# Optimization experiments

Hardware: AMD Instinct MI355X
Metric: run time of the kernel (lower is better)

The kernel has to match this reference:

```python
import jax, jax.numpy as jnp
import numpy as np

# Qwen3MoeSparseMLPBlock config
T = 2048            # tokens
H = 2048            # hidden_size
I = 768             # moe_intermediate_size
E = 32              # num_experts
K = 8               # num_experts_per_tok
CAP = 1024          # per-expert capacity = 2 * (T*K/E); routing is ~uniform so never overflows


def setup_inputs() -> dict:
    key = jax.random.key(0)
    k1, k2, k3, k4, k5 = jax.random.split(key, 5)
    hidden_states = jax.random.normal(k1, (T, H), dtype=jnp.float32)
    gate_w = jax.random.normal(k2, (H, E), dtype=jnp.float32) / np.sqrt(H)
    gate_b = 0.01 * jax.random.normal(k3, (E,), dtype=jnp.float32)
    w_gate_up = jax.random.normal(k4, (E, H, 2 * I), dtype=jnp.float32) / np.sqrt(H)
    w_down = jax.random.normal(k5, (E, I, H), dtype=jnp.float32) / np.sqrt(I)
    return {"hidden_states": hidden_states, "gate_w": gate_w, "gate_b": gate_b,
            "w_gate_up": w_gate_up, "w_down": w_down}


def _moe(x, gate_w, gate_b, w_gate_up, w_down):
    # router: softmax in fp32, top-k, renormalize (norm_topk_prob=True)
    logits = x @ gate_w + gate_b                                   # [T, E]
    probs = jax.nn.softmax(logits.astype(jnp.float32), axis=-1)
    vals, idx = jax.lax.top_k(probs, K)                            # [T, K]
    vals = vals / jnp.sum(vals, axis=-1, keepdims=True)

    # token permutation: sort the T*K (token, expert) assignments by expert id
    A = T * K
    e_flat = idx.reshape(-1)                                       # [A] expert id per assignment
    t_flat = jnp.arange(A, dtype=jnp.int32) // K                   # [A] token id per assignment
    order = jnp.argsort(e_flat)                                    # assignments grouped by expert
    counts = jnp.bincount(e_flat, length=E)                        # [E] tokens per expert
    starts = jnp.cumsum(counts) - counts                           # [E] group offsets

    # fixed-capacity windows into the sorted assignment list (rows beyond count masked)
    win = jnp.minimum(starts[:, None] + jnp.arange(CAP)[None, :], A - 1)   # [E, CAP]
    valid = (jnp.arange(CAP)[None, :] < counts[:, None]).astype(x.dtype)   # [E, CAP]
    tok = t_flat[order][win]                                       # [E, CAP] source token ids
    w = vals.reshape(-1)[order][win] * valid                       # [E, CAP] routing weights (0 on pads)

    # gather -> grouped FFN (SiluAndMul) -> weighted scatter-add combine
    xb = x[tok]                                                    # [E, CAP, H]
    gu = jnp.einsum('ech,ehf->ecf', xb, w_gate_up)                 # [E, CAP, 2I]
    g, u = jnp.split(gu, 2, axis=-1)
    h = jax.nn.silu(g) * u                                         # [E, CAP, I]
    yb = jnp.einsum('eci,eih->ech', h, w_down) * w[..., None]      # [E, CAP, H]
    out = jnp.zeros_like(x).at[tok.reshape(-1)].add(yb.reshape(-1, H))
    return out


def reference(hidden_states, gate_w, gate_b, w_gate_up, w_down):
    return _moe(hidden_states, gate_w, gate_b, w_gate_up, w_down)
```

## Files before the change

### kernel.cpp

```cpp
#include <hip/hip_runtime.h>
#include <math.h>

#define TT 2048
#define HH 2048
#define ID 768
#define NE 32
#define KTOP 8
#define CAP 1024

typedef short bf16x8 __attribute__((ext_vector_type(8)));
typedef float f32x4 __attribute__((ext_vector_type(4)));

__device__ __forceinline__ unsigned short f2b(float f) {
  unsigned int u = __builtin_bit_cast(unsigned int, f);
  u += 0x7fff + ((u >> 16) & 1);
  return (unsigned short)(u >> 16);
}

__global__ __launch_bounds__(256) void cvt_x_kernel(const float* __restrict__ x,
                                                    unsigned short* __restrict__ xb) {
  const size_t i = ((size_t)blockIdx.x * 256 + threadIdx.x) * 8;
  const float4 a = *(const float4*)(x + i);
  const float4 b = *(const float4*)(x + i + 4);
  union { unsigned short us[8]; uint4 v; } p;
  p.us[0] = f2b(a.x); p.us[1] = f2b(a.y); p.us[2] = f2b(a.z); p.us[3] = f2b(a.w);
  p.us[4] = f2b(b.x); p.us[5] = f2b(b.y); p.us[6] = f2b(b.z); p.us[7] = f2b(b.w);
  *(uint4*)(xb + i) = p.v;
}

__global__ __launch_bounds__(256) void router_kernel(
    const float* __restrict__ x, const float* __restrict__ gw,
    const float* __restrict__ gb, int* __restrict__ counts,
    int* __restrict__ tok_slot, float* __restrict__ w_slot) {
  const int t = blockIdx.x;
  const int tid = threadIdx.x;
  const int e = tid & 31;
  const int c = tid >> 5;
  const float* xr = x + (size_t)t * HH;

  __shared__ double pl[8][NE];
  __shared__ float logits[NE];

  double a0 = 0.0, a1 = 0.0, a2 = 0.0, a3 = 0.0;
  const int j0 = c * 256;
#pragma unroll 4
  for (int j = 0; j < 256; j += 4) {
    const int jj = j0 + j;
    a0 = fma((double)xr[jj + 0], (double)gw[(size_t)(jj + 0) * NE + e], a0);
    a1 = fma((double)xr[jj + 1], (double)gw[(size_t)(jj + 1) * NE + e], a1);
    a2 = fma((double)xr[jj + 2], (double)gw[(size_t)(jj + 2) * NE + e], a2);
    a3 = fma((double)xr[jj + 3], (double)gw[(size_t)(jj + 3) * NE + e], a3);
  }
  pl[c][e] = (a0 + a1) + (a2 + a3);
  __syncthreads();

  if (tid < NE) {
    double s = 0.0;
    for (int cc = 0; cc < 8; ++cc) s += pl[cc][tid];
    logits[tid] = (float)s + gb[tid];
  }
  __syncthreads();

  if (tid == 0) {
    float l[NE];
    float m = -1e30f;
    for (int i = 0; i < NE; ++i) { l[i] = logits[i]; m = fmaxf(m, l[i]); }
    int sel[KTOP]; float ex[KTOP]; float s = 0.f;
    for (int k = 0; k < KTOP; ++k) {
      float best = -1e30f; int bi = 0;
      for (int i = 0; i < NE; ++i)
        if (l[i] > best) { best = l[i]; bi = i; }
      sel[k] = bi;
      ex[k] = expf(best - m);
      s += ex[k];
      l[bi] = -1e31f;
    }
    const float inv = 1.f / s;
    for (int k = 0; k < KTOP; ++k) {
      const int ee = sel[k];
      const int pos = atomicAdd(&counts[ee], 1);
      if (pos < CAP) {
        tok_slot[ee * CAP + pos] = t;
        w_slot[ee * CAP + pos] = ex[k] * inv;
      }
    }
  }
}

__global__ __launch_bounds__(256) void gu_kernel(
    const unsigned short* __restrict__ xb, const float* __restrict__ wgu,
    const int* __restrict__ counts, const int* __restrict__ tok_slot,
    unsigned short* __restrict__ h_ws) {
  const int e = blockIdx.z, mt = blockIdx.y, nt = blockIdx.x;
  int cnt = counts[e]; cnt = cnt > CAP ? CAP : cnt;
  if (mt * 128 >= cnt) return;

  __shared__ __align__(16) unsigned short As[128][40];
  __shared__ __align__(16) unsigned short Bg[64][40];
  __shared__ __align__(16) unsigned short Bu[64][40];
  __shared__ int toks[128];

  const int tid = threadIdx.x;
  if (tid < 128) toks[tid] = tok_slot[e * CAP + mt * 128 + tid];
  __syncthreads();

  const float* wg = wgu + (size_t)e * HH * (2 * ID) + nt * 64;
  const float* wu = wg + ID;

  const int wid = tid >> 6, lane = tid & 63;
  const int wm = wid & 1, wn = wid >> 1;
  const int lr = lane & 15, quad = lane >> 4;

  f32x4 accg[4][2], accu[4][2];
  for (int s = 0; s < 4; ++s)
    for (int t = 0; t < 2; ++t)
      for (int r = 0; r < 4; ++r) { accg[s][t][r] = 0.f; accu[s][t][r] = 0.f; }

  for (int k0 = 0; k0 < HH; k0 += 32) {
#pragma unroll
    for (int it = 0; it < 2; ++it) {
      const int task = tid + it * 256;
      const int row = task >> 2, cg = task & 3;
      const uint4 v = *(const uint4*)(xb + (size_t)toks[row] * HH + k0 + cg * 8);
      *(uint4*)&As[row][cg * 8] = v;
    }
#pragma unroll
    for (int it = 0; it < 2; ++it) {
      const int task = tid + it * 256;
      const int k = task >> 4, cg = task & 15;
      const size_t off = (size_t)(k0 + k) * (2 * ID) + cg * 4;
      const float4 vg = *(const float4*)(wg + off);
      const float4 vu = *(const float4*)(wu + off);
      Bg[cg * 4 + 0][k] = f2b(vg.x); Bg[cg * 4 + 1][k] = f2b(vg.y);
      Bg[cg * 4 + 2][k] = f2b(vg.z); Bg[cg * 4 + 3][k] = f2b(vg.w);
      Bu[cg * 4 + 0][k] = f2b(vu.x); Bu[cg * 4 + 1][k] = f2b(vu.y);
      Bu[cg * 4 + 2][k] = f2b(vu.z); Bu[cg * 4 + 3][k] = f2b(vu.w);
    }
    __syncthreads();
    bf16x8 af[4];
#pragma unroll
    for (int s = 0; s < 4; ++s)
      af[s] = *(const bf16x8*)&As[wm * 64 + s * 16 + lr][quad * 8];
#pragma unroll
    for (int t = 0; t < 2; ++t) {
      const bf16x8 bg = *(const bf16x8*)&Bg[wn * 32 + t * 16 + lr][quad * 8];
      const bf16x8 bu = *(const bf16x8*)&Bu[wn * 32 + t * 16 + lr][quad * 8];
#pragma unroll
      for (int s = 0; s < 4; ++s) {
        accg[s][t] = __builtin_amdgcn_mfma_f32_16x16x32_bf16(af[s], bg, accg[s][t], 0, 0, 0);
        accu[s][t] = __builtin_amdgcn_mfma_f32_16x16x32_bf16(af[s], bu, accu[s][t], 0, 0, 0);
      }
    }
    __syncthreads();
  }

  unsigned short* hb = h_ws + (size_t)(e * CAP + mt * 128) * ID + nt * 64;
#pragma unroll
  for (int s = 0; s < 4; ++s)
#pragma unroll
    for (int t = 0; t < 2; ++t)
#pragma unroll
      for (int r = 0; r < 4; ++r) {
        const int row = wm * 64 + s * 16 + quad * 4 + r;
        const int col = wn * 32 + t * 16 + lr;
        const float g = accg[s][t][r], u = accu[s][t][r];
        const float h = (g / (1.f + __expf(-g))) * u;
        hb[(size_t)row * ID + col] = f2b(h);
      }
}

__global__ __launch_bounds__(256) void down_kernel(
    const unsigned short* __restrict__ h_ws, const float* __restrict__ wd,
    const int* __restrict__ counts, const int* __restrict__ tok_slot,
    const float* __restrict__ w_slot, float* __restrict__ out) {
  const int e = blockIdx.z, mt = blockIdx.y;
  const int nb = blockIdx.x * 128;
  int cnt = counts[e]; cnt = cnt > CAP ? CAP : cnt;
  if (mt * 128 >= cnt) return;

  __shared__ __align__(16) unsigned short As[128][40];
  __shared__ __align__(16) unsigned short Bs[128][40];
  __shared__ int toks[128];
  __shared__ float wr[128];

  const int tid = threadIdx.x;
  if (tid < 128) {
    toks[tid] = tok_slot[e * CAP + mt * 128 + tid];
    wr[tid] = w_slot[e * CAP + mt * 128 + tid];
  }

  const unsigned short* hb = h_ws + (size_t)(e * CAP + mt * 128) * ID;
  const float* wb = wd + (size_t)e * ID * HH + nb;

  const int wid = tid >> 6, lane = tid & 63;
  const int wm = wid & 1, wn = wid >> 1;
  const int lr = lane & 15, quad = lane >> 4;

  f32x4 acc[4][4];
  for (int s = 0; s < 4; ++s)
    for (int t = 0; t < 4; ++t)
      for (int r = 0; r < 4; ++r) acc[s][t][r] = 0.f;

  for (int k0 = 0; k0 < ID; k0 += 32) {
#pragma unroll
    for (int it = 0; it < 2; ++it) {
      const int task = tid + it * 256;
      const int row = task >> 2, cg = task & 3;
      const uint4 v = *(const uint4*)(hb + (size_t)row * ID + k0 + cg * 8);
      *(uint4*)&As[row][cg * 8] = v;
    }
#pragma unroll
    for (int it = 0; it < 4; ++it) {
      const int task = tid + it * 256;
      const int k = task >> 5, cg = task & 31;
      const float4 v = *(const float4*)(wb + (size_t)(k0 + k) * HH + cg * 4);
      Bs[cg * 4 + 0][k] = f2b(v.x); Bs[cg * 4 + 1][k] = f2b(v.y);
      Bs[cg * 4 + 2][k] = f2b(v.z); Bs[cg * 4 + 3][k] = f2b(v.w);
    }
    __syncthreads();
    bf16x8 af[4], bfr[4];
#pragma unroll
    for (int s = 0; s < 4; ++s)
      af[s] = *(const bf16x8*)&As[wm * 64 + s * 16 + lr][quad * 8];
#pragma unroll
    for (int t = 0; t < 4; ++t)
      bfr[t] = *(const bf16x8*)&Bs[wn * 64 + t * 16 + lr][quad * 8];
#pragma unroll
    for (int s = 0; s < 4; ++s)
#pragma unroll
      for (int t = 0; t < 4; ++t)
        acc[s][t] = __builtin_amdgcn_mfma_f32_16x16x32_bf16(af[s], bfr[t], acc[s][t], 0, 0, 0);
    __syncthreads();
  }

#pragma unroll
  for (int s = 0; s < 4; ++s) {
#pragma unroll
    for (int r = 0; r < 4; ++r) {
      const int row = wm * 64 + s * 16 + quad * 4 + r;
      const float w = wr[row];
      if (w != 0.f) {
        const int tk = toks[row];
        float* op = out + (size_t)tk * HH + nb + wn * 64 + lr;
#pragma unroll
        for (int t = 0; t < 4; ++t)
          atomicAdd(op + t * 16, acc[s][t][r] * w);
      }
    }
  }
}

extern "C" void kernel_launch(void* const* d_in, const int* in_sizes, int n_in,
                              void* d_out, int out_size, void* d_ws, size_t ws_size,
                              hipStream_t stream) {
  const float* x   = (const float*)d_in[0];
  const float* gw  = (const float*)d_in[1];
  const float* gb  = (const float*)d_in[2];
  const float* wgu = (const float*)d_in[3];
  const float* wd  = (const float*)d_in[4];
  float* out = (float*)d_out;

  char* ws = (char*)d_ws;
  int*   counts   = (int*)ws;
  int*   tok_slot = (int*)(ws + 256);
  float* w_slot   = (float*)(ws + 256 + 131072);
  unsigned short* xb   = (unsigned short*)(ws + 262656);
  unsigned short* h_ws = (unsigned short*)(ws + 262656 + 8388608);

  hipMemsetAsync(d_ws, 0, 262400, stream);
  hipMemsetAsync(d_out, 0, (size_t)out_size * sizeof(float), stream);

  cvt_x_kernel<<<dim3((TT * HH) / (256 * 8)), dim3(256), 0, stream>>>(x, xb);
  router_kernel<<<dim3(TT), dim3(256), 0, stream>>>(x, gw, gb, counts, tok_slot, w_slot);
  gu_kernel<<<dim3(ID / 64, CAP / 128, NE), dim3(256), 0, stream>>>(xb, wgu, counts, tok_slot, h_ws);
  down_kernel<<<dim3(HH / 128, CAP / 128, NE), dim3(256), 0, stream>>>(h_ws, wd, counts, tok_slot, w_slot, out);
}
```

Before: 1.288 ms.

## Pre-transpose weights to bf16 and use direct-to-LDS loads in expert GEMMs

Adds a per-call kernel that converts the fp32 expert weights to bf16 and transposes them to K-contiguous layout in workspace. New gate/up and down GEMM kernels then stage A and B tiles with global_load_lds 16-byte loads, removing per-tile fp32-to-bf16 conversion and register staging. The path only runs when the workspace holds the roughly 360 MB of extra buffers, otherwise the old kernels run. The conversion adds a full pass that reads and writes all weights on every call.

```diff
diff --git a/kernel.cpp b/kernel.cpp
--- a/kernel.cpp
+++ b/kernel.cpp
@@ -15,6 +15,12 @@
   unsigned int u = __builtin_bit_cast(unsigned int, f);
   u += 0x7fff + ((u >> 16) & 1);
   return (unsigned short)(u >> 16);
+}
+
+__device__ __forceinline__ void gload16(const unsigned short* g, void* l) {
+  __builtin_amdgcn_global_load_lds(
+      (const __attribute__((address_space(1))) unsigned int*)g,
+      (__attribute__((address_space(3))) unsigned int*)l, 16, 0, 0);
 }
 
 __global__ __launch_bounds__(256) void cvt_x_kernel(const float* __restrict__ x,
@@ -26,6 +32,35 @@
   p.us[0] = f2b(a.x); p.us[1] = f2b(a.y); p.us[2] = f2b(a.z); p.us[3] = f2b(a.w);
   p.us[4] = f2b(b.x); p.us[5] = f2b(b.y); p.us[6] = f2b(b.z); p.us[7] = f2b(b.w);
   *(uint4*)(xb + i) = p.v;
+}
+
+__global__ __launch_bounds__(256) void cvt_w_kernel(const float* __restrict__ in,
+                                                    unsigned short* __restrict__ out,
+                                                    int R, int C) {
+  __shared__ float tile[64][65];
+  const int e = blockIdx.z;
+  const int r0 = blockIdx.y * 64, c0 = blockIdx.x * 64;
+  const int tid = threadIdx.x;
+  const float* src = in + (size_t)e * R * C;
+  const int rr = tid >> 4, c4 = tid & 15;
+#pragma unroll
+  for (int it = 0; it < 4; ++it) {
+    const int r = it * 16 + rr;
+    const float4 v = *(const float4*)(src + (size_t)(r0 + r) * C + c0 + c4 * 4);
+    tile[r][c4 * 4 + 0] = v.x; tile[r][c4 * 4 + 1] = v.y;
+    tile[r][c4 * 4 + 2] = v.z; tile[r][c4 * 4 + 3] = v.w;
+  }
+  __syncthreads();
+  unsigned short* dst = out + (size_t)e * R * C;
+#pragma unroll
+  for (int it = 0; it < 2; ++it) {
+    const int task = tid + it * 256;
+    const int c = task >> 3, g = task & 7;
+    union { unsigned short us[8]; uint4 v; } p;
+#pragma unroll
+    for (int j = 0; j < 8; ++j) p.us[j] = f2b(tile[g * 8 + j][c]);
+    *(uint4*)(dst + (size_t)(c0 + c) * R + r0 + g * 8) = p.v;
+  }
 }
 
 __global__ __launch_bounds__(256) void router_kernel(
@@ -87,6 +122,168 @@
   }
 }
 
+
+__global__ __launch_bounds__(256) void gu2_kernel(
+    const unsigned short* __restrict__ xb, const unsigned short* __restrict__ wguT,
+    const int* __restrict__ counts, const int* __restrict__ tok_slot,
+    unsigned short* __restrict__ h_ws) {
+  const int e = blockIdx.z, mt = blockIdx.y, nt = blockIdx.x;
+  int cnt = counts[e]; cnt = cnt > CAP ? CAP : cnt;
+  if (mt * 128 >= cnt) return;
+
+  __shared__ __align__(16) unsigned short As[128 * 32];
+  __shared__ __align__(16) unsigned short Bg[64 * 32];
+  __shared__ __align__(16) unsigned short Bu[64 * 32];
+  __shared__ int toks[128];
+
+  const int tid = threadIdx.x;
+  if (tid < 128) toks[tid] = tok_slot[e * CAP + mt * 128 + tid];
+  __syncthreads();
+
+  const unsigned short* bgp = wguT + (size_t)e * (2 * ID) * HH + (size_t)(nt * 64) * HH;
+  const unsigned short* bup = bgp + (size_t)ID * HH;
+
+  const int wv = tid >> 6;
+  const int ar = tid >> 2, cg = tid & 3;
+  char* ldsA0 = (char*)As + wv * 1024;
+  char* ldsA1 = (char*)As + 4096 + wv * 1024;
+  char* ldsBg = (char*)Bg + wv * 1024;
+  char* ldsBu = (char*)Bu + wv * 1024;
+  const unsigned short* srcA0 = xb + (size_t)toks[ar] * HH + cg * 8;
+  const unsigned short* srcA1 = xb + (size_t)toks[ar + 64] * HH + cg * 8;
+  const unsigned short* srcBg = bgp + (size_t)ar * HH + cg * 8;
+  const unsigned short* srcBu = bup + (size_t)ar * HH + cg * 8;
+
+  const int wid = tid >> 6, lane = tid & 63;
+  const int wm = wid & 1, wn = wid >> 1;
+  const int lr = lane & 15, quad = lane >> 4;
+
+  f32x4 accg[4][2], accu[4][2];
+  for (int s = 0; s < 4; ++s)
+    for (int t = 0; t < 2; ++t)
+      for (int r = 0; r < 4; ++r) { accg[s][t][r] = 0.f; accu[s][t][r] = 0.f; }
+
+  for (int k0 = 0; k0 < HH; k0 += 32) {
+    gload16(srcA0 + k0, ldsA0);
+    gload16(srcA1 + k0, ldsA1);
+    gload16(srcBg + k0, ldsBg);
+    gload16(srcBu + k0, ldsBu);
+    __syncthreads();
+    bf16x8 af[4];
+#pragma unroll
+    for (int s = 0; s < 4; ++s)
+      af[s] = *(const bf16x8*)&As[(wm * 64 + s * 16 + lr) * 32 + quad * 8];
+#pragma unroll
+    for (int t = 0; t < 2; ++t) {
+      const bf16x8 bg = *(const bf16x8*)&Bg[(wn * 32 + t * 16 + lr) * 32 + quad * 8];
+      const bf16x8 bu = *(const bf16x8*)&Bu[(wn * 32 + t * 16 + lr) * 32 + quad * 8];
+#pragma unroll
+      for (int s = 0; s < 4; ++s) {
+        accg[s][t] = __builtin_amdgcn_mfma_f32_16x16x32_bf16(af[s], bg, accg[s][t], 0, 0, 0);
+        accu[s][t] = __builtin_amdgcn_mfma_f32_16x16x32_bf16(af[s], bu, accu[s][t], 0, 0, 0);
+      }
+    }
+    __syncthreads();
+  }
+
+  unsigned short* hb = h_ws + (size_t)(e * CAP + mt * 128) * ID + nt * 64;
+#pragma unroll
+  for (int s = 0; s < 4; ++s)
+#pragma unroll
+    for (int t = 0; t < 2; ++t)
+#pragma unroll
+      for (int r = 0; r < 4; ++r) {
+        const int row = wm * 64 + s * 16 + quad * 4 + r;
+        const int col = wn * 32 + t * 16 + lr;
+        const float g = accg[s][t][r], u = accu[s][t][r];
+        const float h = (g / (1.f + __expf(-g))) * u;
+        hb[(size_t)row * ID + col] = f2b(h);
+      }
+}
+
+__global__ __launch_bounds__(256) void down2_kernel(
+    const unsigned short* __restrict__ h_ws, const unsigned short* __restrict__ wdT,
+    const int* __restrict__ counts, const int* __restrict__ tok_slot,
+    const float* __restrict__ w_slot, float* __restrict__ out) {
+  const int e = blockIdx.z, mt = blockIdx.y;
+  const int nb = blockIdx.x * 128;
+  int cnt = counts[e]; cnt = cnt > CAP ? CAP : cnt;
+  if (mt * 128 >= cnt) return;
+
+  __shared__ __align__(16) unsigned short As[128 * 32];
+  __shared__ __align__(16) unsigned short Bs[128 * 32];
+  __shared__ int toks[128];
+  __shared__ float wr[128];
+
+  const int tid = threadIdx.x;
+  if (tid < 128) {
+    toks[tid] = tok_slot[e * CAP + mt * 128 + tid];
+    wr[tid] = w_slot[e * CAP + mt * 128 + tid];
+  }
+  __syncthreads();
+
+  const unsigned short* hb = h_ws + (size_t)(e * CAP + mt * 128) * ID;
+  const unsigned short* wb = wdT + (size_t)e * HH * ID + (size_t)nb * ID;
+
+  const int wv = tid >> 6;
+  const int ar = tid >> 2, cg = tid & 3;
+  char* ldsA0 = (char*)As + wv * 1024;
+  char* ldsA1 = (char*)As + 4096 + wv * 1024;
+  char* ldsB0 = (char*)Bs + wv * 1024;
+  char* ldsB1 = (char*)Bs + 4096 + wv * 1024;
+  const unsigned short* srcA0 = hb + (size_t)ar * ID + cg * 8;
+  const unsigned short* srcA1 = hb + (size_t)(ar + 64) * ID + cg * 8;
+  const unsigned short* srcB0 = wb + (size_t)ar * ID + cg * 8;
+  const unsigned short* srcB1 = wb + (size_t)(ar + 64) * ID + cg * 8;
+
+  const int wid = tid >> 6, lane = tid & 63;
+  const int wm = wid & 1, wn = wid >> 1;
+  const int lr = lane & 15, quad = lane >> 4;
+
+  f32x4 acc[4][4];
+  for (int s = 0; s < 4; ++s)
+    for (int t = 0; t < 4; ++t)
+      for (int r = 0; r < 4; ++r) acc[s][t][r] = 0.f;
+
+  for (int k0 = 0; k0 < ID; k0 += 32) {
+    gload16(srcA0 + k0, ldsA0);
+    gload16(srcA1 + k0, ldsA1);
+    gload16(srcB0 + k0, ldsB0);
+    gload16(srcB1 + k0, ldsB1);
+    __syncthreads();
+    bf16x8 af[4], bfr[4];
+#pragma unroll
+    for (int s = 0; s < 4; ++s)
+      af[s] = *(const bf16x8*)&As[(wm * 64 + s * 16 + lr) * 32 + quad * 8];
+#pragma unroll
+    for (int t = 0; t < 4; ++t)
+      bfr[t] = *(const bf16x8*)&Bs[(wn * 64 + t * 16 + lr) * 32 + quad * 8];
+#pragma unroll
+    for (int s = 0; s < 4; ++s)
+#pragma unroll
+      for (int t = 0; t < 4; ++t)
+        acc[s][t] = __builtin_amdgcn_mfma_f32_16x16x32_bf16(af[s], bfr[t], acc[s][t], 0, 0, 0);
+    __syncthreads();
+  }
+
+#pragma unroll
+  for (int s = 0; s < 4; ++s) {
+#pragma unroll
+    for (int r = 0; r < 4; ++r) {
+      const int row = wm * 64 + s * 16 + quad * 4 + r;
+      const float w = wr[row];
+      if (w != 0.f) {
+        const int tk = toks[row];
+        float* op = out + (size_t)tk * HH + nb + wn * 64 + lr;
+#pragma unroll
+        for (int t = 0; t < 4; ++t)
+          atomicAdd(op + t * 16, acc[s][t][r] * w);
+      }
+    }
+  }
+}
+
+
 __global__ __launch_bounds__(256) void gu_kernel(
     const unsigned short* __restrict__ xb, const float* __restrict__ wgu,
     const int* __restrict__ counts, const int* __restrict__ tok_slot,
@@ -265,13 +462,24 @@
   int*   tok_slot = (int*)(ws + 256);
   float* w_slot   = (float*)(ws + 256 + 131072);
   unsigned short* xb   = (unsigned short*)(ws + 262656);
-  unsigned short* h_ws = (unsigned short*)(ws + 262656 + 8388608);
+  unsigned short* h_ws = (unsigned short*)(ws + 8651264);
+  unsigned short* wguT = (unsigned short*)(ws + 58982912);
+  unsigned short* wdT  = (unsigned short*)(ws + 260309504);
+  const size_t NEED = 360972800ULL;
 
   hipMemsetAsync(d_ws, 0, 262400, stream);
   hipMemsetAsync(d_out, 0, (size_t)out_size * sizeof(float), stream);
 
   cvt_x_kernel<<<dim3((TT * HH) / (256 * 8)), dim3(256), 0, stream>>>(x, xb);
   router_kernel<<<dim3(TT), dim3(256), 0, stream>>>(x, gw, gb, counts, tok_slot, w_slot);
-  gu_kernel<<<dim3(ID / 64, CAP / 128, NE), dim3(256), 0, stream>>>(xb, wgu, counts, tok_slot, h_ws);
-  down_kernel<<<dim3(HH / 128, CAP / 128, NE), dim3(256), 0, stream>>>(h_ws, wd, counts, tok_slot, w_slot, out);
-}
+
+  if (ws_size >= NEED) {
+    cvt_w_kernel<<<dim3((2 * ID) / 64, HH / 64, NE), dim3(256), 0, stream>>>(wgu, wguT, HH, 2 * ID);
+    cvt_w_kernel<<<dim3(HH / 64, ID / 64, NE), dim3(256), 0, stream>>>(wd, wdT, ID, HH);
+    gu2_kernel<<<dim3(ID / 64, CAP / 128, NE), dim3(256), 0, stream>>>(xb, wguT, counts, tok_slot, h_ws);
+    down2_kernel<<<dim3(HH / 128, CAP / 128, NE), dim3(256), 0, stream>>>(h_ws, wdT, counts, tok_slot, w_slot, out);
+  } else {
+    gu_kernel<<<dim3(ID / 64, CAP / 128, NE), dim3(256), 0, stream>>>(xb, wgu, counts, tok_slot, h_ws);
+    down_kernel<<<dim3(HH / 128, CAP / 128, NE), dim3(256), 0, stream>>>(h_ws, wd, counts, tok_slot, w_slot, out);
+  }
+}
```

Result: faster. 1.146 ms (-11.0%).
